# Performance work log

Measured on AMD Instinct MI355X. Metric: run time of the kernel, lower is better.

Reference implementation:

```python
import jax, jax.numpy as jnp
import numpy as np

B, N, D, K = 128, 512, 512, 8

def setup_inputs() -> dict:
    key = jax.random.key(0)
    ks = jax.random.split(key, 6)
    coefficients = jax.random.normal(ks[0], (B, N, D), dtype=jnp.float32)
    H = D // 2
    s1 = 1.0 / np.sqrt(D)
    s2 = 1.0 / np.sqrt(H)
    W1 = jax.random.uniform(ks[1], (D, H), jnp.float32, -s1, s1)
    b1 = jax.random.uniform(ks[2], (H,), jnp.float32, -s1, s1)
    W2 = jax.random.uniform(ks[3], (H,), jnp.float32, -s2, s2)
    b2 = jax.random.uniform(ks[4], (), jnp.float32, -s2, s2)
    base_logits = jnp.zeros((N,), jnp.float32)  # nn.Parameter(torch.zeros(n_freqs))
    return {"coefficients": coefficients, "W1": W1, "b1": b1, "W2": W2, "b2": b2,
            "base_logits": base_logits}

def reference(coefficients, W1, b1, W2, b2, base_logits):
    # scorer: Linear(D, D//2) -> GELU(exact) -> Linear(D//2, 1), squeeze last dim
    h = jax.nn.gelu(jnp.einsum('bnd,dh->bnh', coefficients, W1) + b1, approximate=False)
    logits = jnp.einsum('bnh,h->bn', h, W2) + b2 + base_logits[None, :]  # (B, N)
    # inference path (self.training == False): plain softmax, no gumbel noise
    probs = jax.nn.softmax(logits, axis=-1)
    _, indices = jax.lax.top_k(probs, K)                      # (B, K) int32
    mask = jnp.zeros_like(probs).at[jnp.arange(B)[:, None], indices].set(1.0)
    selected = jnp.take_along_axis(coefficients, indices[:, :, None], axis=1)  # (B, K, D)
    importance = probs  # softmax(logits) again in torch; identical in eval mode
    return selected, mask, importance, indices
```

## Files before the change

### kernel.cpp

```cpp
#include <hip/hip_runtime.h>
#include <math.h>

#define B_DIM 128
#define N_DIM 512
#define D_DIM 512
#define H_DIM 256
#define K_SEL 8

typedef __bf16 bf16x8 __attribute__((ext_vector_type(8)));
typedef float  f32x4  __attribute__((ext_vector_type(4)));

__device__ __forceinline__ void gload_lds16(const void* g, void* l) {
    __builtin_amdgcn_global_load_lds((const __attribute__((address_space(1))) void*)g,
                                     (__attribute__((address_space(3))) void*)l, 16, 0, 0);
}

__global__ __launch_bounds__(256) void prep_w1_kernel(
    const float* __restrict__ W1,
    __bf16* __restrict__ w1t_h,
    __bf16* __restrict__ w1t_m,
    __bf16* __restrict__ w1t_l)
{
    const int c = blockIdx.x;
    const int t = threadIdx.x;
    #pragma unroll
    for (int kk = 0; kk < D_DIM; kk += 256) {
        int k = kk + t;
        float x = W1[(size_t)k * H_DIM + c];
        __bf16 h = (__bf16)x;
        float r1 = x - (float)h;
        __bf16 m = (__bf16)r1;
        float r2 = r1 - (float)m;
        __bf16 l = (__bf16)r2;
        w1t_h[(size_t)c * D_DIM + k] = h;
        w1t_m[(size_t)c * D_DIM + k] = m;
        w1t_l[(size_t)c * D_DIM + k] = l;
    }
}

__global__ __launch_bounds__(512, 2) void fused_scorer_mfma(
    const float* __restrict__ X,
    const __bf16* __restrict__ w1t_h,
    const __bf16* __restrict__ w1t_m,
    const __bf16* __restrict__ w1t_l,
    const float* __restrict__ b1,
    const float* __restrict__ W2,
    const float* __restrict__ b2p,
    const float* __restrict__ base_logits,
    float* __restrict__ logits)
{
    __shared__ bf16x8 Ah[2][512], Am[2][512], Al[2][512];
    __shared__ bf16x8 Bh[2][1024], Bm[2][1024], Bl[2][1024];
    __shared__ float red[4][128];

    const int tid  = threadIdx.x;
    const int lane = tid & 63;
    const int wave = tid >> 6;
    const int wm   = (wave >> 2) << 6;
    const int wn   = (wave & 3) << 6;
    const int l15  = lane & 15;
    const int lg   = lane >> 4;
    const int row0 = blockIdx.x * 128;

    const float* xp = X + (size_t)(row0 + (tid & 127)) * D_DIM + (tid >> 7) * 8;
    const int bcol = tid & 255;
    const int bk1  = (tid >> 8) * 8;
    const int bk2  = bk1 + 16;

    f32x4 acc[4][4];
    #pragma unroll
    for (int mi = 0; mi < 4; ++mi)
        #pragma unroll
        for (int nj = 0; nj < 4; ++nj)
            acc[mi][nj] = (f32x4){0.f, 0.f, 0.f, 0.f};

    float b1v[4], w2v[4];
    #pragma unroll
    for (int nj = 0; nj < 4; ++nj) {
        int col = wn + nj * 16 + l15;
        b1v[nj] = b1[col];
        w2v[nj] = W2[col];
    }

    auto split_write = [&](int buf, float4 va, float4 vb) {
        float e[8] = {va.x, va.y, va.z, va.w, vb.x, vb.y, vb.z, vb.w};
        bf16x8 hh, mm, ll;
        #pragma unroll
        for (int j = 0; j < 8; ++j) {
            float x = e[j];
            __bf16 h = (__bf16)x;
            float r1 = x - (float)h;
            __bf16 m = (__bf16)r1;
            float r2 = r1 - (float)m;
            hh[j] = h; mm[j] = m; ll[j] = (__bf16)r2;
        }
        Ah[buf][tid] = hh;
        Am[buf][tid] = mm;
        Al[buf][tid] = ll;
    };
    auto stage_b = [&](int buf, int kc) {
        size_t s1 = (size_t)bcol * D_DIM + kc + bk1;
        size_t s2 = (size_t)bcol * D_DIM + kc + bk2;
        gload_lds16(w1t_h + s1, &Bh[buf][tid]);
        gload_lds16(w1t_h + s2, &Bh[buf][tid + 512]);
        gload_lds16(w1t_m + s1, &Bm[buf][tid]);
        gload_lds16(w1t_m + s2, &Bm[buf][tid + 512]);
        gload_lds16(w1t_l + s1, &Bl[buf][tid]);
        gload_lds16(w1t_l + s2, &Bl[buf][tid + 512]);
    };

    float4 xa = *reinterpret_cast<const float4*>(xp);
    float4 xb = *reinterpret_cast<const float4*>(xp + 4);
    stage_b(0, 0);
    split_write(0, xa, xb);
    xa = *reinterpret_cast<const float4*>(xp + 32);
    xb = *reinterpret_cast<const float4*>(xp + 36);
    __syncthreads();

    for (int ks = 0; ks < 16; ++ks) {
        const int buf = ks & 1, nbuf = buf ^ 1;
        stage_b(nbuf, ((ks + 1) * 32) & 511);
        split_write(nbuf, xa, xb);
        const int k2 = ((ks + 2) * 32) & 511;
        xa = *reinterpret_cast<const float4*>(xp + k2);
        xb = *reinterpret_cast<const float4*>(xp + k2 + 4);
        bf16x8 fah[4], fam[4], fal[4], fbh[4], fbm[4], fbl[4];
        #pragma unroll
        for (int mi = 0; mi < 4; ++mi) {
            int ca = lg * 128 + wm + mi * 16 + l15;
            fah[mi] = Ah[buf][ca];
            fam[mi] = Am[buf][ca];
            fal[mi] = Al[buf][ca];
        }
        #pragma unroll
        for (int nj = 0; nj < 4; ++nj) {
            int cb = lg * 256 + wn + nj * 16 + l15;
            fbh[nj] = Bh[buf][cb];
            fbm[nj] = Bm[buf][cb];
            fbl[nj] = Bl[buf][cb];
        }
        #pragma unroll
        for (int mi = 0; mi < 4; ++mi)
            #pragma unroll
            for (int nj = 0; nj < 4; ++nj) {
                acc[mi][nj] = __builtin_amdgcn_mfma_f32_16x16x32_bf16(fah[mi], fbh[nj], acc[mi][nj], 0, 0, 0);
                acc[mi][nj] = __builtin_amdgcn_mfma_f32_16x16x32_bf16(fah[mi], fbm[nj], acc[mi][nj], 0, 0, 0);
                acc[mi][nj] = __builtin_amdgcn_mfma_f32_16x16x32_bf16(fam[mi], fbh[nj], acc[mi][nj], 0, 0, 0);
                acc[mi][nj] = __builtin_amdgcn_mfma_f32_16x16x32_bf16(fah[mi], fbl[nj], acc[mi][nj], 0, 0, 0);
                acc[mi][nj] = __builtin_amdgcn_mfma_f32_16x16x32_bf16(fam[mi], fbm[nj], acc[mi][nj], 0, 0, 0);
                acc[mi][nj] = __builtin_amdgcn_mfma_f32_16x16x32_bf16(fal[mi], fbh[nj], acc[mi][nj], 0, 0, 0);
            }
        __syncthreads();
    }

    float part[4][4];
    #pragma unroll
    for (int mi = 0; mi < 4; ++mi)
        #pragma unroll
        for (int r = 0; r < 4; ++r)
            part[mi][r] = 0.f;
    #pragma unroll
    for (int mi = 0; mi < 4; ++mi)
        #pragma unroll
        for (int nj = 0; nj < 4; ++nj)
            #pragma unroll
            for (int r = 0; r < 4; ++r) {
                float z = acc[mi][nj][r] + b1v[nj];
                float g = 0.5f * z * (1.0f + erff(z * 0.70710678118654752440f));
                part[mi][r] = fmaf(g, w2v[nj], part[mi][r]);
            }
    #pragma unroll
    for (int mi = 0; mi < 4; ++mi)
        #pragma unroll
        for (int r = 0; r < 4; ++r) {
            float v = part[mi][r];
            v += __shfl_xor(v, 1, 16);
            v += __shfl_xor(v, 2, 16);
            v += __shfl_xor(v, 4, 16);
            v += __shfl_xor(v, 8, 16);
            if (l15 == 0)
                red[wave & 3][wm + mi * 16 + lg * 4 + r] = v;
        }
    __syncthreads();
    if (tid < 128) {
        float s = red[0][tid] + red[1][tid] + red[2][tid] + red[3][tid];
        int grow = row0 + tid;
        logits[grow] = s + b2p[0] + base_logits[grow & (N_DIM - 1)];
    }
}

__global__ __launch_bounds__(256) void softmax_topk_kernel(
    const float* __restrict__ logits,
    float* __restrict__ out_mask,
    float* __restrict__ out_importance,
    float* __restrict__ out_indices)
{
    const int b = blockIdx.x;
    const int tid = threadIdx.x;
    __shared__ float probs[N_DIM];
    __shared__ float redf[4];
    __shared__ int   redi[4];
    __shared__ int   sel_idx[K_SEL];

    float l0 = logits[b * N_DIM + tid];
    float l1 = logits[b * N_DIM + tid + 256];

    float m = fmaxf(l0, l1);
    #pragma unroll
    for (int s = 32; s >= 1; s >>= 1) m = fmaxf(m, __shfl_xor(m, s, 64));
    if ((tid & 63) == 0) redf[tid >> 6] = m;
    __syncthreads();
    float gm = fmaxf(fmaxf(redf[0], redf[1]), fmaxf(redf[2], redf[3]));
    __syncthreads();

    float e0 = expf(l0 - gm), e1 = expf(l1 - gm);
    float ssum = e0 + e1;
    #pragma unroll
    for (int s = 32; s >= 1; s >>= 1) ssum += __shfl_xor(ssum, s, 64);
    if ((tid & 63) == 0) redf[tid >> 6] = ssum;
    __syncthreads();
    float denom = redf[0] + redf[1] + redf[2] + redf[3];
    float p0 = e0 / denom, p1 = e1 / denom;
    probs[tid] = p0;
    probs[tid + 256] = p1;
    out_importance[b * N_DIM + tid] = p0;
    out_importance[b * N_DIM + tid + 256] = p1;
    __syncthreads();

    for (int it = 0; it < K_SEL; ++it) {
        float v0 = probs[tid]; int i0 = tid;
        float v1 = probs[tid + 256];
        if (v1 > v0) { v0 = v1; i0 = tid + 256; }
        #pragma unroll
        for (int s = 32; s >= 1; s >>= 1) {
            float ov = __shfl_xor(v0, s, 64);
            int   oi = __shfl_xor(i0, s, 64);
            if (ov > v0 || (ov == v0 && oi < i0)) { v0 = ov; i0 = oi; }
        }
        if ((tid & 63) == 0) { redf[tid >> 6] = v0; redi[tid >> 6] = i0; }
        __syncthreads();
        if (tid == 0) {
            float bv = redf[0]; int bi = redi[0];
            for (int w = 1; w < 4; ++w)
                if (redf[w] > bv || (redf[w] == bv && redi[w] < bi)) { bv = redf[w]; bi = redi[w]; }
            sel_idx[it] = bi;
            probs[bi] = -1.0f;
        }
        __syncthreads();
    }

    float mk0 = 0.f, mk1 = 0.f;
    #pragma unroll
    for (int i = 0; i < K_SEL; ++i) {
        if (sel_idx[i] == tid)       mk0 = 1.f;
        if (sel_idx[i] == tid + 256) mk1 = 1.f;
    }
    out_mask[b * N_DIM + tid] = mk0;
    out_mask[b * N_DIM + tid + 256] = mk1;

    if (tid < K_SEL) out_indices[b * K_SEL + tid] = (float)sel_idx[tid];
}

__global__ __launch_bounds__(256) void gather_kernel(
    const float* __restrict__ X,
    const float* __restrict__ out_indices,
    float* __restrict__ out_selected)
{
    const int b = blockIdx.x;
    const int tid = threadIdx.x;
    __shared__ int sel[K_SEL];
    if (tid < K_SEL) sel[tid] = (int)out_indices[b * K_SEL + tid];
    __syncthreads();
    #pragma unroll
    for (int i = 0; i < 4; ++i) {
        int f = tid + 256 * i;
        int ki = f >> 7;
        int c4 = f & 127;
        float4 v = reinterpret_cast<const float4*>(
            X + ((size_t)b * N_DIM + sel[ki]) * D_DIM)[c4];
        reinterpret_cast<float4*>(
            out_selected + ((size_t)b * K_SEL + ki) * D_DIM)[c4] = v;
    }
}

extern "C" void kernel_launch(void* const* d_in, const int* in_sizes, int n_in,
                              void* d_out, int out_size, void* d_ws, size_t ws_size,
                              hipStream_t stream) {
    const float* X           = (const float*)d_in[0];
    const float* W1          = (const float*)d_in[1];
    const float* b1          = (const float*)d_in[2];
    const float* W2          = (const float*)d_in[3];
    const float* b2          = (const float*)d_in[4];
    const float* base_logits = (const float*)d_in[5];

    float* out            = (float*)d_out;
    float* out_selected   = out;
    float* out_mask       = out_selected + B_DIM * K_SEL * D_DIM;
    float* out_importance = out_mask + B_DIM * N_DIM;
    float* out_indices    = out_importance + B_DIM * N_DIM;

    float*  logits = out_selected;
    __bf16* w1t_h  = (__bf16*)(out_selected + 65536);
    __bf16* w1t_m  = (__bf16*)(out_selected + 131072);
    __bf16* w1t_l  = (__bf16*)(out_selected + 196608);

    hipLaunchKernelGGL(prep_w1_kernel, dim3(H_DIM), dim3(256), 0, stream,
                       W1, w1t_h, w1t_m, w1t_l);
    hipLaunchKernelGGL(fused_scorer_mfma, dim3((B_DIM * N_DIM) / 128), dim3(512), 0, stream,
                       X, w1t_h, w1t_m, w1t_l, b1, W2, b2, base_logits, logits);
    hipLaunchKernelGGL(softmax_topk_kernel, dim3(B_DIM), dim3(256), 0, stream,
                       logits, out_mask, out_importance, out_indices);
    hipLaunchKernelGGL(gather_kernel, dim3(B_DIM), dim3(256), 0, stream,
                       X, out_indices, out_selected);
}
```

Baseline: 133.3 us.

## Replace 3-way bf16 split GEMM with 2-way scaled fp16 split and smaller tiles

Switches the emulated-fp32 GEMM from a three-term bf16 split (six MFMAs per tile) to a two-term fp16 split with a 2048-scaled residual (three MFMAs per tile), accumulating the correction terms separately. It also moves from 128-row blocks of 512 threads to 64-row blocks of 256 threads, adds an XOR swizzle on the A tile in LDS, and reuses the A buffer for the final reduction. This cuts MFMA work and LDS/global traffic for the weight copies. The cost is somewhat lower precision and fp16 range limits, which could change top-k selection on close logits.

```diff
diff --git a/kernel.cpp b/kernel.cpp
--- a/kernel.cpp
+++ b/kernel.cpp
@@ -7,8 +7,8 @@
 #define H_DIM 256
 #define K_SEL 8
 
-typedef __bf16 bf16x8 __attribute__((ext_vector_type(8)));
-typedef float  f32x4  __attribute__((ext_vector_type(4)));
+typedef _Float16 half8 __attribute__((ext_vector_type(8)));
+typedef float    f32x4 __attribute__((ext_vector_type(4)));
 
 __device__ __forceinline__ void gload_lds16(const void* g, void* l) {
     __builtin_amdgcn_global_load_lds((const __attribute__((address_space(1))) void*)g,
@@ -17,9 +17,8 @@
 
 __global__ __launch_bounds__(256) void prep_w1_kernel(
     const float* __restrict__ W1,
-    __bf16* __restrict__ w1t_h,
-    __bf16* __restrict__ w1t_m,
-    __bf16* __restrict__ w1t_l)
+    _Float16* __restrict__ w1t_h,
+    _Float16* __restrict__ w1t_l)
 {
     const int c = blockIdx.x;
     const int t = threadIdx.x;
@@ -27,52 +26,46 @@
     for (int kk = 0; kk < D_DIM; kk += 256) {
         int k = kk + t;
         float x = W1[(size_t)k * H_DIM + c];
-        __bf16 h = (__bf16)x;
-        float r1 = x - (float)h;
-        __bf16 m = (__bf16)r1;
-        float r2 = r1 - (float)m;
-        __bf16 l = (__bf16)r2;
+        _Float16 h = (_Float16)x;
+        float r = x - (float)h;
         w1t_h[(size_t)c * D_DIM + k] = h;
-        w1t_m[(size_t)c * D_DIM + k] = m;
-        w1t_l[(size_t)c * D_DIM + k] = l;
-    }
-}
-
-__global__ __launch_bounds__(512, 2) void fused_scorer_mfma(
+        w1t_l[(size_t)c * D_DIM + k] = (_Float16)(r * 2048.0f);
+    }
+}
+
+__global__ __launch_bounds__(256, 2) void fused_scorer_mfma(
     const float* __restrict__ X,
-    const __bf16* __restrict__ w1t_h,
-    const __bf16* __restrict__ w1t_m,
-    const __bf16* __restrict__ w1t_l,
+    const _Float16* __restrict__ w1t_h,
+    const _Float16* __restrict__ w1t_l,
     const float* __restrict__ b1,
     const float* __restrict__ W2,
     const float* __restrict__ b2p,
     const float* __restrict__ base_logits,
     float* __restrict__ logits)
 {
-    __shared__ bf16x8 Ah[2][512], Am[2][512], Al[2][512];
-    __shared__ bf16x8 Bh[2][1024], Bm[2][1024], Bl[2][1024];
-    __shared__ float red[4][128];
+    __shared__ half8 Ah[2][256], Al[2][256];
+    __shared__ half8 Bh[2][1024], Bl[2][1024];
 
     const int tid  = threadIdx.x;
     const int lane = tid & 63;
     const int wave = tid >> 6;
-    const int wm   = (wave >> 2) << 6;
-    const int wn   = (wave & 3) << 6;
+    const int wn   = wave << 6;
     const int l15  = lane & 15;
     const int lg   = lane >> 4;
-    const int row0 = blockIdx.x * 128;
-
-    const float* xp = X + (size_t)(row0 + (tid & 127)) * D_DIM + (tid >> 7) * 8;
-    const int bcol = tid & 255;
-    const int bk1  = (tid >> 8) * 8;
-    const int bk2  = bk1 + 16;
-
-    f32x4 acc[4][4];
+    const int row0 = blockIdx.x * 64;
+
+    const int rowA = tid >> 2, kcA = tid & 3;
+    const float* xp = X + (size_t)(row0 + rowA) * D_DIM + kcA * 8;
+    const int achunk_sw = (kcA * 64 + rowA) ^ (kcA << 1);
+
+    f32x4 acc[4][4], acc2[4][4];
     #pragma unroll
     for (int mi = 0; mi < 4; ++mi)
         #pragma unroll
-        for (int nj = 0; nj < 4; ++nj)
-            acc[mi][nj] = (f32x4){0.f, 0.f, 0.f, 0.f};
+        for (int nj = 0; nj < 4; ++nj) {
+            acc[mi][nj]  = (f32x4){0.f, 0.f, 0.f, 0.f};
+            acc2[mi][nj] = (f32x4){0.f, 0.f, 0.f, 0.f};
+        }
 
     float b1v[4], w2v[4];
     #pragma unroll
@@ -84,29 +77,25 @@
 
     auto split_write = [&](int buf, float4 va, float4 vb) {
         float e[8] = {va.x, va.y, va.z, va.w, vb.x, vb.y, vb.z, vb.w};
-        bf16x8 hh, mm, ll;
+        half8 hh, ll;
         #pragma unroll
         for (int j = 0; j < 8; ++j) {
-            float x = e[j];
-            __bf16 h = (__bf16)x;
-            float r1 = x - (float)h;
-            __bf16 m = (__bf16)r1;
-            float r2 = r1 - (float)m;
-            hh[j] = h; mm[j] = m; ll[j] = (__bf16)r2;
-        }
-        Ah[buf][tid] = hh;
-        Am[buf][tid] = mm;
-        Al[buf][tid] = ll;
+            _Float16 h = (_Float16)e[j];
+            float r = e[j] - (float)h;
+            hh[j] = h;
+            ll[j] = (_Float16)(r * 2048.0f);
+        }
+        Ah[buf][achunk_sw] = hh;
+        Al[buf][achunk_sw] = ll;
     };
-    auto stage_b = [&](int buf, int kc) {
-        size_t s1 = (size_t)bcol * D_DIM + kc + bk1;
-        size_t s2 = (size_t)bcol * D_DIM + kc + bk2;
-        gload_lds16(w1t_h + s1, &Bh[buf][tid]);
-        gload_lds16(w1t_h + s2, &Bh[buf][tid + 512]);
-        gload_lds16(w1t_m + s1, &Bm[buf][tid]);
-        gload_lds16(w1t_m + s2, &Bm[buf][tid + 512]);
-        gload_lds16(w1t_l + s1, &Bl[buf][tid]);
-        gload_lds16(w1t_l + s2, &Bl[buf][tid + 512]);
+    auto stage_b = [&](int buf, int kc0) {
+        const _Float16* sh = w1t_h + (size_t)tid * D_DIM + kc0;
+        const _Float16* sl = w1t_l + (size_t)tid * D_DIM + kc0;
+        #pragma unroll
+        for (int q = 0; q < 4; ++q) {
+            gload_lds16(sh + q * 8, &Bh[buf][q * 256 + tid]);
+            gload_lds16(sl + q * 8, &Bl[buf][q * 256 + tid]);
+        }
     };
 
     float4 xa = *reinterpret_cast<const float4*>(xp);
@@ -124,35 +113,32 @@
         const int k2 = ((ks + 2) * 32) & 511;
         xa = *reinterpret_cast<const float4*>(xp + k2);
         xb = *reinterpret_cast<const float4*>(xp + k2 + 4);
-        bf16x8 fah[4], fam[4], fal[4], fbh[4], fbm[4], fbl[4];
+
+        half8 fah[4], fal[4], fbh[4], fbl[4];
         #pragma unroll
         for (int mi = 0; mi < 4; ++mi) {
-            int ca = lg * 128 + wm + mi * 16 + l15;
+            int ca = (lg * 64 + mi * 16 + l15) ^ (lg << 1);
             fah[mi] = Ah[buf][ca];
-            fam[mi] = Am[buf][ca];
             fal[mi] = Al[buf][ca];
         }
         #pragma unroll
         for (int nj = 0; nj < 4; ++nj) {
             int cb = lg * 256 + wn + nj * 16 + l15;
             fbh[nj] = Bh[buf][cb];
-            fbm[nj] = Bm[buf][cb];
             fbl[nj] = Bl[buf][cb];
         }
         #pragma unroll
         for (int mi = 0; mi < 4; ++mi)
             #pragma unroll
             for (int nj = 0; nj < 4; ++nj) {
-                acc[mi][nj] = __builtin_amdgcn_mfma_f32_16x16x32_bf16(fah[mi], fbh[nj], acc[mi][nj], 0, 0, 0);
-                acc[mi][nj] = __builtin_amdgcn_mfma_f32_16x16x32_bf16(fah[mi], fbm[nj], acc[mi][nj], 0, 0, 0);
-                acc[mi][nj] = __builtin_amdgcn_mfma_f32_16x16x32_bf16(fam[mi], fbh[nj], acc[mi][nj], 0, 0, 0);
-                acc[mi][nj] = __builtin_amdgcn_mfma_f32_16x16x32_bf16(fah[mi], fbl[nj], acc[mi][nj], 0, 0, 0);
-                acc[mi][nj] = __builtin_amdgcn_mfma_f32_16x16x32_bf16(fam[mi], fbm[nj], acc[mi][nj], 0, 0, 0);
-                acc[mi][nj] = __builtin_amdgcn_mfma_f32_16x16x32_bf16(fal[mi], fbh[nj], acc[mi][nj], 0, 0, 0);
+                acc[mi][nj]  = __builtin_amdgcn_mfma_f32_16x16x32_f16(fah[mi], fbh[nj], acc[mi][nj],  0, 0, 0);
+                acc2[mi][nj] = __builtin_amdgcn_mfma_f32_16x16x32_f16(fah[mi], fbl[nj], acc2[mi][nj], 0, 0, 0);
+                acc2[mi][nj] = __builtin_amdgcn_mfma_f32_16x16x32_f16(fal[mi], fbh[nj], acc2[mi][nj], 0, 0, 0);
             }
         __syncthreads();
     }
 
+    float* red = reinterpret_cast<float*>(&Ah[0][0]);
     float part[4][4];
     #pragma unroll
     for (int mi = 0; mi < 4; ++mi)
@@ -165,7 +151,7 @@
         for (int nj = 0; nj < 4; ++nj)
             #pragma unroll
             for (int r = 0; r < 4; ++r) {
-                float z = acc[mi][nj][r] + b1v[nj];
+                float z = acc[mi][nj][r] + acc2[mi][nj][r] * (1.0f / 2048.0f) + b1v[nj];
                 float g = 0.5f * z * (1.0f + erff(z * 0.70710678118654752440f));
                 part[mi][r] = fmaf(g, w2v[nj], part[mi][r]);
             }
@@ -179,11 +165,11 @@
             v += __shfl_xor(v, 4, 16);
             v += __shfl_xor(v, 8, 16);
             if (l15 == 0)
-                red[wave & 3][wm + mi * 16 + lg * 4 + r] = v;
-        }
-    __syncthreads();
-    if (tid < 128) {
-        float s = red[0][tid] + red[1][tid] + red[2][tid] + red[3][tid];
+                red[wave * 64 + mi * 16 + lg * 4 + r] = v;
+        }
+    __syncthreads();
+    if (tid < 64) {
+        float s = red[tid] + red[64 + tid] + red[128 + tid] + red[192 + tid];
         int grow = row0 + tid;
         logits[grow] = s + b2p[0] + base_logits[grow & (N_DIM - 1)];
     }
@@ -299,15 +285,14 @@
     float* out_importance = out_mask + B_DIM * N_DIM;
     float* out_indices    = out_importance + B_DIM * N_DIM;
 
-    float*  logits = out_selected;
-    __bf16* w1t_h  = (__bf16*)(out_selected + 65536);
-    __bf16* w1t_m  = (__bf16*)(out_selected + 131072);
-    __bf16* w1t_l  = (__bf16*)(out_selected + 196608);
+    float*    logits = out_selected;
+    _Float16* w1t_h  = (_Float16*)(out_selected + 65536);
+    _Float16* w1t_l  = (_Float16*)(out_selected + 131072);
 
     hipLaunchKernelGGL(prep_w1_kernel, dim3(H_DIM), dim3(256), 0, stream,
-                       W1, w1t_h, w1t_m, w1t_l);
-    hipLaunchKernelGGL(fused_scorer_mfma, dim3((B_DIM * N_DIM) / 128), dim3(512), 0, stream,
-                       X, w1t_h, w1t_m, w1t_l, b1, W2, b2, base_logits, logits);
+                       W1, w1t_h, w1t_l);
+    hipLaunchKernelGGL(fused_scorer_mfma, dim3((B_DIM * N_DIM) / 64), dim3(256), 0, stream,
+                       X, w1t_h, w1t_l, b1, W2, b2, base_logits, logits);
     hipLaunchKernelGGL(softmax_topk_kernel, dim3(B_DIM), dim3(256), 0, stream,
                        logits, out_mask, out_importance, out_indices);
     hipLaunchKernelGGL(gather_kernel, dim3(B_DIM), dim3(256), 0, stream,
```

New measurement: 158.8 us. 19.2% more time.
